# Performance work log

Hardware: AMD Instinct MI355X
Metric: run time of the kernel (lower is better)

The kernel has to match this reference:

```python
import jax, jax.numpy as jnp
import numpy as np

B, C, CI, H, W = 8, 256, 128, 64, 64
STD = 0.01  # conv_init_std
EPS = 1e-5


def setup_inputs() -> dict:
    key = jax.random.key(0)
    ks = jax.random.split(key, 6)
    return {
        "x": jax.random.normal(ks[0], (B, C, H, W), dtype=jnp.float32),
        "theta_w": jax.random.normal(ks[1], (CI, C), dtype=jnp.float32) * STD,
        "theta_b": jnp.zeros((CI,), jnp.float32),
        "phi_w": jax.random.normal(ks[2], (CI, C), dtype=jnp.float32) * STD,
        "phi_b": jnp.zeros((CI,), jnp.float32),
        "g_w": jax.random.normal(ks[3], (CI, C), dtype=jnp.float32) * STD,
        "g_b": jnp.zeros((CI,), jnp.float32),
        "wz_w": jax.random.normal(ks[4], (C, CI), dtype=jnp.float32) * STD,
        "wz_b": jnp.zeros((C,), jnp.float32),
        "bn_gamma": jnp.ones((C,), jnp.float32),
        "bn_beta": jnp.zeros((C,), jnp.float32),
    }


def _conv1x1(x, w, b):
    # 1x1 conv == channel matmul: (B,Cin,H,W),(Cout,Cin) -> (B,Cout,H,W)
    return jnp.einsum('bchw,oc->bohw', x, w) + b[None, :, None, None]


def reference(x, theta_w, theta_b, phi_w, phi_b, g_w, g_b, wz_w, wz_b, bn_gamma, bn_beta):
    b, c, h, w = x.shape
    ci = theta_w.shape[0]
    # query over full resolution: (B, CI, N) with N = H*W
    theta = _conv1x1(x, theta_w, theta_b).reshape(b, ci, h * w)
    # 2x2 maxpool stride 2 for key/value inputs
    xp = x.reshape(b, c, h // 2, 2, w // 2, 2).max(axis=(3, 5))
    phi = _conv1x1(xp, phi_w, phi_b).reshape(b, ci, -1)   # (B, CI, N')
    g = _conv1x1(xp, g_w, g_b).reshape(b, ci, -1)         # (B, CI, N')
    # scaled dot-product attention: scores (B, N, N')
    scores = jnp.einsum('bcn,bcm->bnm', theta, phi) * (ci ** -0.5)
    p = jax.nn.softmax(scores, axis=-1)
    t = jnp.einsum('bcm,bnm->bcn', g, p).reshape(b, ci, h, w)
    z = _conv1x1(t, wz_w, wz_b)
    # BatchNorm2d, training-mode batch statistics (biased variance)
    mean = z.mean(axis=(0, 2, 3))
    var = z.var(axis=(0, 2, 3))
    z = (z - mean[None, :, None, None]) * jax.lax.rsqrt(var + EPS)[None, :, None, None]
    z = z * bn_gamma[None, :, None, None] + bn_beta[None, :, None, None]
    return x + z
```

## Files before the change

### kernel.cpp

```cpp
#include <hip/hip_runtime.h>

#define B_   8
#define C_   256
#define CI_  128
#define HW_  4096
#define HWP_ 1024

typedef short bf16x8 __attribute__((ext_vector_type(8)));
typedef float f32x4 __attribute__((ext_vector_type(4)));
typedef unsigned short u16;
typedef unsigned int u32;

#define SW(row, off) ((off) ^ (((row) & 7) << 4))

__device__ __forceinline__ u16 f2b(float f) {
  u32 u = __builtin_bit_cast(u32, f);
  return (u16)((u + 0x7fffu + ((u >> 16) & 1u)) >> 16);
}
__device__ __forceinline__ u32 cvtpk(float lo, float hi) {
  u32 r;
  asm("v_cvt_pk_bf16_f32 %0, %1, %2" : "=v"(r) : "v"(lo), "v"(hi));
  return r;
}
__device__ __forceinline__ f32x4 mfma16(bf16x8 a, bf16x8 b, f32x4 c) {
  return __builtin_amdgcn_mfma_f32_16x16x32_bf16(a, b, c, 0, 0, 0);
}
__device__ __forceinline__ void gl16(const void* g, void* l) {
  __builtin_amdgcn_global_load_lds(
      (const __attribute__((address_space(1))) u32*)g,
      (__attribute__((address_space(3))) u32*)l, 16, 0, 0);
}

template <int ROWS>
__device__ __forceinline__ void stage_tile(const u16* src, int rstride,
                                           char* lds, int w, int lane) {
#pragma unroll
  for (int it = 0; it < ROWS / 32; ++it) {
    int L = it * 256 + w * 64 + lane;
    int row = L >> 3, slot = L & 7;
    gl16(src + (size_t)row * rstride + ((slot ^ (row & 7)) << 3),
         lds + it * 4096 + w * 1024);
  }
}
__device__ __forceinline__ void stage_tile256(const u16* src, char* lds, int w, int lane) {
#pragma unroll
  for (int it = 0; it < 4; ++it) {
    int L = it * 256 + w * 64 + lane;
    int row = L >> 4, slot = L & 15;
    gl16(src + (size_t)row * 128 + ((slot ^ (row & 7)) << 3),
         lds + it * 4096 + w * 1024);
  }
}

__global__ __launch_bounds__(256) void prep(const float* __restrict__ x,
                                            u16* __restrict__ xt,
                                            u16* __restrict__ xpt,
                                            const float* __restrict__ w0,
                                            const float* __restrict__ w1,
                                            const float* __restrict__ w2,
                                            const float* __restrict__ w3,
                                            u16* __restrict__ wB) {
  const int b = blockIdx.z, p = blockIdx.x;
  const int t = threadIdx.x;
  if (p == 32) {
    if (blockIdx.y == 0 && b < 4) {
      const float* src = (b == 0) ? w0 : (b == 1) ? w1 : (b == 2) ? w2 : w3;
      u16* dst = wB + b * 32768;
      for (int i = t * 8; i < 32768; i += 2048) {
        float4 a = *(const float4*)&src[i];
        float4 c = *(const float4*)&src[i + 4];
        uint4 v;
        v.x = cvtpk(a.x, a.y);
        v.y = cvtpk(a.z, a.w);
        v.z = cvtpk(c.x, c.y);
        v.w = cvtpk(c.z, c.w);
        *(uint4*)&dst[i] = v;
      }
    }
    return;
  }
  __shared__ __align__(16) char sm[16384];
  const int c0 = blockIdx.y * 64;
#pragma unroll
  for (int k = 0; k < 2; ++k) {
    int pi = k * 256 + t;
    int ng = pi & 31, cg = pi >> 5;
    float4 v[4];
#pragma unroll
    for (int cc = 0; cc < 4; ++cc)
      v[cc] = *(const float4*)&x[((size_t)(b * C_ + c0 + cg * 4 + cc)) * HW_ + p * 128 + ng * 4];
#pragma unroll
    for (int jj = 0; jj < 4; ++jj) {
      int n = ng * 4 + jj;
      uint2 pk;
      pk.x = cvtpk(v[0][jj], v[1][jj]);
      pk.y = cvtpk(v[2][jj], v[3][jj]);
      int slot = (cg + ng) & 15;
      *(uint2*)(sm + n * 128 + slot * 8) = pk;
    }
  }
  __syncthreads();
#pragma unroll
  for (int it = 0; it < 4; ++it) {
    int L = it * 256 + t;
    int row = L >> 3, ch = L & 7;
    int s0 = (2 * ch + (row >> 2)) & 15, s1 = (2 * ch + 1 + (row >> 2)) & 15;
    uint2 a = *(const uint2*)(sm + row * 128 + s0 * 8);
    uint2 bb = *(const uint2*)(sm + row * 128 + s1 * 8);
    uint4 o = {a.x, a.y, bb.x, bb.y};
    *(uint4*)(xt + ((size_t)(b * HW_ + p * 128 + row)) * C_ + c0 + ch * 8) = o;
  }
#pragma unroll
  for (int k = 0; k < 2; ++k) {
    int cg = t & 15, mw = (t >> 4) + k * 16;
    int rows[4] = {2 * mw, 2 * mw + 1, 64 + 2 * mw, 65 + 2 * mw};
    uint2 rv[4];
#pragma unroll
    for (int r = 0; r < 4; ++r) {
      int n = rows[r];
      int slot = (cg + (n >> 2)) & 15;
      rv[r] = *(const uint2*)(sm + n * 128 + slot * 8);
    }
    u16 outc[4];
#pragma unroll
    for (int ci = 0; ci < 4; ++ci) {
      float m = -1e30f;
#pragma unroll
      for (int r = 0; r < 4; ++r) {
        u32 word = (ci < 2) ? rv[r].x : rv[r].y;
        u16 h = (u16)((ci & 1) ? (word >> 16) : (word & 0xffff));
        m = fmaxf(m, __builtin_bit_cast(float, (u32)h << 16));
      }
      outc[ci] = (u16)(__builtin_bit_cast(u32, m) >> 16);
    }
    uint2 pk;
    pk.x = (u32)outc[0] | ((u32)outc[1] << 16);
    pk.y = (u32)outc[2] | ((u32)outc[3] << 16);
    *(uint2*)(xpt + ((size_t)(b * HWP_ + p * 32 + mw)) * C_ + c0 + cg * 4) = pk;
  }
}

__global__ __launch_bounds__(256) void gemm_wa(const u16* __restrict__ Wb,
                                               const u16* __restrict__ act,
                                               const float* __restrict__ bias,
                                               u16* __restrict__ outp,
                                               int Ntok) {
  __shared__ __align__(16) char smem[65536];
  const int b = blockIdx.y;
  const int n0 = blockIdx.x * 128;
  const int t = threadIdx.x, lane = t & 63, w = t >> 6;
  const int lr = lane & 15, lg = lane >> 4;
  const int otb = (w & 1) * 4, ntb = (w >> 1) * 4;
  const u16* actb = act + (size_t)(b * Ntok + n0) * 256;
  f32x4 acc[4][4];
#pragma unroll
  for (int i = 0; i < 4; ++i)
#pragma unroll
    for (int j = 0; j < 4; ++j) acc[i][j] = (f32x4){0.f, 0.f, 0.f, 0.f};

  stage_tile<128>(Wb, 256, smem, w, lane);
  stage_tile<128>(actb, 256, smem + 16384, w, lane);
  for (int kc = 0; kc < 4; ++kc) {
    __syncthreads();
    if (kc < 3) {
      char* nb = smem + ((kc + 1) & 1) * 32768;
      stage_tile<128>(Wb + (kc + 1) * 64, 256, nb, w, lane);
      stage_tile<128>(actb + (kc + 1) * 64, 256, nb + 16384, w, lane);
    }
    char* Ws = smem + (kc & 1) * 32768;
    char* Xs = Ws + 16384;
#pragma unroll
    for (int ks = 0; ks < 2; ++ks) {
      bf16x8 af[4], bfr[4];
#pragma unroll
      for (int i = 0; i < 4; ++i) {
        int rA = (otb + i) * 16 + lr;
        af[i] = *(const bf16x8*)(Ws + rA * 128 + SW(rA, ks * 64 + lg * 16));
        int rB = (ntb + i) * 16 + lr;
        bfr[i] = *(const bf16x8*)(Xs + rB * 128 + SW(rB, ks * 64 + lg * 16));
      }
#pragma unroll
      for (int i = 0; i < 4; ++i)
#pragma unroll
        for (int j = 0; j < 4; ++j) acc[i][j] = mfma16(af[i], bfr[j], acc[i][j]);
    }
  }
#pragma unroll
  for (int i = 0; i < 4; ++i) {
    int obase = (otb + i) * 16 + lg * 4;
    float b0 = bias[obase], b1 = bias[obase + 1], b2 = bias[obase + 2], b3 = bias[obase + 3];
#pragma unroll
    for (int j = 0; j < 4; ++j) {
      int n = (ntb + j) * 16 + lr;
      f32x4 v = acc[i][j];
      uint2 pk;
      pk.x = cvtpk(v[0] + b0, v[1] + b1);
      pk.y = cvtpk(v[2] + b2, v[3] + b3);
      *(uint2*)(smem + n * 256 + SW(n, obase * 2)) = pk;
    }
  }
  __syncthreads();
#pragma unroll
  for (int it = 0; it < 8; ++it) {
    int L = it * 256 + t;
    int row = L >> 4, ch = L & 15;
    uint4 v = *(const uint4*)(smem + row * 256 + SW(row, ch * 16));
    *(uint4*)(outp + ((size_t)b * Ntok + n0 + row) * 128 + ch * 8) = v;
  }
}

template <int KD, bool BNP>
__global__ __launch_bounds__(256) void gemm_aw(const u16* __restrict__ act,
                                               const u16* __restrict__ Wb,
                                               const float* __restrict__ bias,
                                               u16* __restrict__ outp,
                                               int Mtok, int O,
                                               float* __restrict__ sums,
                                               float* __restrict__ sqs) {
  __shared__ __align__(16) char smem[49152];
  const int b = blockIdx.z;
  const int m0 = blockIdx.x * 64;
  const int o0 = blockIdx.y * 128;
  const int t = threadIdx.x, lane = t & 63, w = t >> 6;
  const int lr = lane & 15, lg = lane >> 4;
  const int otb = w * 2;
  const u16* actb = act + (size_t)(b * Mtok + m0) * KD;
  const u16* Wbb = Wb + (size_t)o0 * KD;
  constexpr int NCH = KD / 64;
  f32x4 acc[4][2];
#pragma unroll
  for (int i = 0; i < 4; ++i)
#pragma unroll
    for (int j = 0; j < 2; ++j) acc[i][j] = (f32x4){0.f, 0.f, 0.f, 0.f};

  stage_tile<64>(actb, KD, smem, w, lane);
  stage_tile<128>(Wbb, KD, smem + 8192, w, lane);
  for (int kc = 0; kc < NCH; ++kc) {
    __syncthreads();
    if (kc < NCH - 1) {
      char* nb = smem + ((kc + 1) & 1) * 24576;
      stage_tile<64>(actb + (kc + 1) * 64, KD, nb, w, lane);
      stage_tile<128>(Wbb + (kc + 1) * 64, KD, nb + 8192, w, lane);
    }
    char* As = smem + (kc & 1) * 24576;
    char* Bs = As + 8192;
#pragma unroll
    for (int ks = 0; ks < 2; ++ks) {
      bf16x8 af[4], bfr[2];
#pragma unroll
      for (int i = 0; i < 4; ++i) {
        int r = i * 16 + lr;
        af[i] = *(const bf16x8*)(As + r * 128 + SW(r, ks * 64 + lg * 16));
      }
#pragma unroll
      for (int j = 0; j < 2; ++j) {
        int r = (otb + j) * 16 + lr;
        bfr[j] = *(const bf16x8*)(Bs + r * 128 + SW(r, ks * 64 + lg * 16));
      }
#pragma unroll
      for (int i = 0; i < 4; ++i)
#pragma unroll
        for (int j = 0; j < 2; ++j) acc[i][j] = mfma16(af[i], bfr[j], acc[i][j]);
    }
  }
  if (BNP) {
    int pid = blockIdx.z * gridDim.x + blockIdx.x;
#pragma unroll
    for (int j = 0; j < 2; ++j) {
      int o = o0 + (otb + j) * 16 + lr;
      float bi = bias[o];
      float s = 0.f, q = 0.f;
#pragma unroll
      for (int i = 0; i < 4; ++i) {
        f32x4 v = acc[i][j];
#pragma unroll
        for (int r = 0; r < 4; ++r) {
          float vv = v[r] + bi;
          s += vv;
          q += vv * vv;
        }
      }
      s += __shfl_xor(s, 16); q += __shfl_xor(q, 16);
      s += __shfl_xor(s, 32); q += __shfl_xor(q, 32);
      if (lg == 0) {
        sums[(size_t)o * 512 + pid] = s;
        sqs[(size_t)o * 512 + pid] = q;
      }
    }
  }
#pragma unroll
  for (int j = 0; j < 2; ++j) {
    int o = (otb + j) * 16 + lr;
    float bi = bias[o0 + o];
#pragma unroll
    for (int i = 0; i < 4; ++i) {
      int mq = i * 16 + lg * 4;
      f32x4 v = acc[i][j];
      uint2 pk;
      pk.x = cvtpk(v[0] + bi, v[1] + bi);
      pk.y = cvtpk(v[2] + bi, v[3] + bi);
      *(uint2*)(smem + o * 128 + SW(o, mq * 2)) = pk;
    }
  }
  __syncthreads();
#pragma unroll
  for (int it = 0; it < 4; ++it) {
    int L = it * 256 + t;
    int row = L >> 3, ch = L & 7;
    uint4 v = *(const uint4*)(smem + row * 128 + SW(row, ch * 16));
    *(uint4*)(outp + ((size_t)b * O + o0 + row) * Mtok + m0 + ch * 8) = v;
  }
}

#define ATTN_TILE(KCP, WAITV)                                                 \
  {                                                                           \
    const char* Kc = (KCP);                                                   \
    int rn = w * 16 + lr;                                                     \
    _Pragma("unroll")                                                         \
    for (int mt = 0; mt < 4; ++mt) {                                          \
      f32x4 s = {0.f, 0.f, 0.f, 0.f};                                         \
      _Pragma("unroll")                                                       \
      for (int kq = 0; kq < 4; ++kq) {                                        \
        int r = mt * 16 + lr;                                                 \
        bf16x8 a = *(const bf16x8*)(Kc + r * 256 + SW(r, kq * 64 + lg * 16)); \
        s = mfma16(a, qf[kq], s);                                             \
      }                                                                       \
      float p0 = __expf(s[0] * scale), p1 = __expf(s[1] * scale);             \
      float p2 = __expf(s[2] * scale), p3 = __expf(s[3] * scale);             \
      csum += (p0 + p1) + (p2 + p3);                                          \
      uint2 pk;                                                               \
      pk.x = cvtpk(p0, p1);                                                   \
      pk.y = cvtpk(p2, p3);                                                   \
      *(uint2*)(Pn + rn * 128 + SW(rn, mt * 32 + lg * 8)) = pk;               \
    }                                                                         \
    asm volatile("s_waitcnt lgkmcnt(0)" ::: "memory");                        \
    bf16x8 pb0 = *(const bf16x8*)(Pn + rn * 128 + SW(rn, lg * 16));           \
    bf16x8 pb1 = *(const bf16x8*)(Pn + rn * 128 + SW(rn, 64 + lg * 16));      \
    asm volatile("s_waitcnt " WAITV ::: "memory");                            \
    _Pragma("unroll")                                                         \
    for (int ct = 0; ct < 8; ++ct) {                                          \
      int rc = ct * 16 + lr;                                                  \
      bf16x8 a0 = *(const bf16x8*)(Vs + rc * 128 + SW(rc, lg * 16));          \
      bf16x8 a1 = *(const bf16x8*)(Vs + rc * 128 + SW(rc, 64 + lg * 16));     \
      accT[ct] = mfma16(a0, pb0, accT[ct]);                                   \
      accT[ct] = mfma16(a1, pb1, accT[ct]);                                   \
    }                                                                         \
  }

__global__ __launch_bounds__(256) void attn_mfma(const u16* __restrict__ Qt,
                                                 const u16* __restrict__ Kt,
                                                 const u16* __restrict__ Vn,
                                                 u16* __restrict__ Ot) {
  __shared__ __align__(16) char smem[73728];
  char* Vs = smem + 49152;
  char* Pn = smem + 65536;
  const int bid = blockIdx.x;
  const int swz = (bid & 7) * 64 + (bid >> 3);
  const int b = swz >> 6, n0 = (swz & 63) * 64;
  const int t = threadIdx.x, lane = t & 63, w = t >> 6;
  const int lr = lane & 15, lg = lane >> 4;
  const float scale = 0.08838834764831845f;
  const u16* Qbase = Qt + (size_t)(b * HW_ + n0) * 128;
  const u16* Kbase = Kt + (size_t)b * HWP_ * 128;
  const u16* Vbase = Vn + (size_t)b * 128 * HWP_;

  stage_tile256(Qbase, smem, w, lane);
  stage_tile256(Kbase, smem + 16384, w, lane);
  stage_tile<128>(Vbase, HWP_, Vs, w, lane);
  __syncthreads();

  bf16x8 qf[4];
  {
    int r = w * 16 + lr;
#pragma unroll
    for (int kq = 0; kq < 4; ++kq)
      qf[kq] = *(const bf16x8*)(smem + r * 256 + SW(r, kq * 64 + lg * 16));
  }
  f32x4 accT[8];
#pragma unroll
  for (int ct = 0; ct < 8; ++ct) accT[ct] = (f32x4){0.f, 0.f, 0.f, 0.f};
  float csum = 0.f;

  for (int tt = 0; tt < 15; ++tt) {
    stage_tile256(Kbase + (size_t)(tt + 1) * 64 * 128,
                  smem + 16384 + ((tt + 1) & 1) * 16384, w, lane);
    ATTN_TILE(smem + 16384 + (tt & 1) * 16384, "vmcnt(4)");
    __syncthreads();
    stage_tile<128>(Vbase + (tt + 1) * 64, HWP_, Vs, w, lane);
  }
  ATTN_TILE(smem + 16384 + 16384, "vmcnt(0)");

  csum += __shfl_xor(csum, 16);
  csum += __shfl_xor(csum, 32);
  float rinv = 1.f / csum;
  __syncthreads();
  {
    int rn = w * 16 + lr;
#pragma unroll
    for (int ct = 0; ct < 8; ++ct) {
      f32x4 v = accT[ct];
      uint2 pk;
      pk.x = cvtpk(v[0] * rinv, v[1] * rinv);
      pk.y = cvtpk(v[2] * rinv, v[3] * rinv);
      *(uint2*)(smem + 16384 + rn * 256 + SW(rn, ct * 32 + lg * 8)) = pk;
    }
  }
  __syncthreads();
#pragma unroll
  for (int it = 0; it < 4; ++it) {
    int L = it * 256 + t;
    int row = L >> 4, ch = L & 15;
    uint4 v = *(const uint4*)(smem + 16384 + row * 256 + SW(row, ch * 16));
    *(uint4*)(Ot + ((size_t)b * HW_ + n0 + row) * 128 + ch * 8) = v;
  }
}

__global__ __launch_bounds__(256) void bn_finalize(const float* __restrict__ sums,
                                                   const float* __restrict__ sqs,
                                                   float* __restrict__ stats) {
  __shared__ float s1[256], s2[256];
  const int c = blockIdx.x, t = threadIdx.x;
  float a = sums[(size_t)c * 512 + t] + sums[(size_t)c * 512 + 256 + t];
  float q = sqs[(size_t)c * 512 + t] + sqs[(size_t)c * 512 + 256 + t];
  s1[t] = a;
  s2[t] = q;
  __syncthreads();
  for (int st = 128; st > 0; st >>= 1) {
    if (t < st) {
      s1[t] += s1[t + st];
      s2[t] += s2[t + st];
    }
    __syncthreads();
  }
  if (t == 0) {
    const float inv = 1.f / (float)(B_ * HW_);
    float mean = s1[0] * inv;
    float var = s2[0] * inv - mean * mean;
    stats[c] = mean;
    stats[C_ + c] = rsqrtf(var + 1e-5f);
  }
}

__device__ __forceinline__ float blo(u32 u) { return __builtin_bit_cast(float, u << 16); }
__device__ __forceinline__ float bhi(u32 u) { return __builtin_bit_cast(float, u & 0xffff0000u); }

__global__ __launch_bounds__(256) void final8(const float4* __restrict__ x,
                                              const uint4* __restrict__ zb,
                                              const float* __restrict__ stats,
                                              const float* __restrict__ gamma,
                                              const float* __restrict__ beta,
                                              float4* __restrict__ out) {
  size_t i = (size_t)blockIdx.x * 256 + threadIdx.x;
  int c = (int)((i >> 9) & 255);
  float ga = gamma[c] * stats[C_ + c];
  float be = beta[c] - stats[c] * ga;
  uint4 zv = zb[i];
  float4 x0 = x[2 * i], x1 = x[2 * i + 1], o0, o1;
  o0.x = fmaf(blo(zv.x), ga, x0.x + be);
  o0.y = fmaf(bhi(zv.x), ga, x0.y + be);
  o0.z = fmaf(blo(zv.y), ga, x0.z + be);
  o0.w = fmaf(bhi(zv.y), ga, x0.w + be);
  o1.x = fmaf(blo(zv.z), ga, x1.x + be);
  o1.y = fmaf(bhi(zv.z), ga, x1.y + be);
  o1.z = fmaf(blo(zv.w), ga, x1.z + be);
  o1.w = fmaf(bhi(zv.w), ga, x1.w + be);
  out[2 * i] = o0;
  out[2 * i + 1] = o1;
}

extern "C" void kernel_launch(void* const* d_in, const int* in_sizes, int n_in,
                              void* d_out, int out_size, void* d_ws, size_t ws_size,
                              hipStream_t stream) {
  const float* x        = (const float*)d_in[0];
  const float* theta_w  = (const float*)d_in[1];
  const float* theta_b  = (const float*)d_in[2];
  const float* phi_w    = (const float*)d_in[3];
  const float* phi_b    = (const float*)d_in[4];
  const float* g_w      = (const float*)d_in[5];
  const float* g_b      = (const float*)d_in[6];
  const float* wz_w     = (const float*)d_in[7];
  const float* wz_b     = (const float*)d_in[8];
  const float* bn_gamma = (const float*)d_in[9];
  const float* bn_beta  = (const float*)d_in[10];
  float* out = (float*)d_out;

  char* ws = (char*)d_ws;
  u16* x_t     = (u16*)(ws);
  u16* xp_t    = (u16*)(ws + 16777216);
  u16* theta_t = (u16*)(ws + 20971520);
  u16* phi_t   = (u16*)(ws + 29360128);
  u16* g_nat   = (u16*)(ws + 31457280);
  u16* t_t     = (u16*)(ws + 33554432);
  u16* zb      = (u16*)(ws + 41943040);
  float* stats = (float*)(ws + 58720256);
  float* bsums = (float*)(ws + 58722304);
  float* bsqs  = (float*)(ws + 59246592);
  u16* wB      = (u16*)(ws + 59770880);

  prep<<<dim3(33, 4, 8), 256, 0, stream>>>(x, x_t, xp_t, theta_w, phi_w, g_w, wz_w, wB);
  gemm_wa<<<dim3(32, 8), 256, 0, stream>>>(wB, x_t, theta_b, theta_t, HW_);
  gemm_wa<<<dim3(8, 8), 256, 0, stream>>>(wB + 32768, xp_t, phi_b, phi_t, HWP_);
  gemm_aw<256, false><<<dim3(16, 1, 8), 256, 0, stream>>>(
      xp_t, wB + 65536, g_b, g_nat, HWP_, 128, nullptr, nullptr);
  attn_mfma<<<dim3(512), 256, 0, stream>>>(theta_t, phi_t, g_nat, t_t);
  gemm_aw<128, true><<<dim3(64, 2, 8), 256, 0, stream>>>(
      t_t, wB + 98304, wz_b, zb, HW_, 256, bsums, bsqs);
  bn_finalize<<<256, 256, 0, stream>>>(bsums, bsqs, stats);
  final8<<<4096, 256, 0, stream>>>((const float4*)x, (const uint4*)zb, stats,
                                   bn_gamma, bn_beta, (float4*)out);
}
```

Before: 169.1 us.

## Fuse theta projection and output conv with BN partial sums into attention kernel

The theta 1x1 conv is now computed inside the attention kernel from the bf16 x tile staged in LDS. The wz output conv and the per-block BatchNorm partial sums are applied to the attention output while it is still in LDS. This drops two GEMM launches and the global round trips for theta and t. In exchange the attention kernel does more work per block and uses more registers (launch bounds set to 2 blocks per CU), and it reloads weight tiles in every block.

After: 160.1 us. -5.3%, faster.

```diff
diff --git a/kernel.cpp b/kernel.cpp
--- a/kernel.cpp
+++ b/kernel.cpp
@@ -48,6 +48,15 @@
     int L = it * 256 + w * 64 + lane;
     int row = L >> 4, slot = L & 15;
     gl16(src + (size_t)row * 128 + ((slot ^ (row & 7)) << 3),
+         lds + it * 4096 + w * 1024);
+  }
+}
+__device__ __forceinline__ void stage512(const u16* src, char* lds, int w, int lane) {
+#pragma unroll
+  for (int it = 0; it < 8; ++it) {
+    int L = it * 256 + w * 64 + lane;
+    int row = L >> 5, slot = L & 31;
+    gl16(src + (size_t)row * 256 + ((slot ^ (row & 7)) << 3),
          lds + it * 4096 + w * 1024);
   }
 }
@@ -209,14 +218,12 @@
   }
 }
 
-template <int KD, bool BNP>
+template <int KD>
 __global__ __launch_bounds__(256) void gemm_aw(const u16* __restrict__ act,
                                                const u16* __restrict__ Wb,
                                                const float* __restrict__ bias,
                                                u16* __restrict__ outp,
-                                               int Mtok, int O,
-                                               float* __restrict__ sums,
-                                               float* __restrict__ sqs) {
+                                               int Mtok, int O) {
   __shared__ __align__(16) char smem[49152];
   const int b = blockIdx.z;
   const int m0 = blockIdx.x * 64;
@@ -261,31 +268,6 @@
       for (int i = 0; i < 4; ++i)
 #pragma unroll
         for (int j = 0; j < 2; ++j) acc[i][j] = mfma16(af[i], bfr[j], acc[i][j]);
-    }
-  }
-  if (BNP) {
-    int pid = blockIdx.z * gridDim.x + blockIdx.x;
-#pragma unroll
-    for (int j = 0; j < 2; ++j) {
-      int o = o0 + (otb + j) * 16 + lr;
-      float bi = bias[o];
-      float s = 0.f, q = 0.f;
-#pragma unroll
-      for (int i = 0; i < 4; ++i) {
-        f32x4 v = acc[i][j];
-#pragma unroll
-        for (int r = 0; r < 4; ++r) {
-          float vv = v[r] + bi;
-          s += vv;
-          q += vv * vv;
-        }
-      }
-      s += __shfl_xor(s, 16); q += __shfl_xor(q, 16);
-      s += __shfl_xor(s, 32); q += __shfl_xor(q, 32);
-      if (lg == 0) {
-        sums[(size_t)o * 512 + pid] = s;
-        sqs[(size_t)o * 512 + pid] = q;
-      }
     }
   }
 #pragma unroll
@@ -347,11 +329,15 @@
     }                                                                         \
   }
 
-__global__ __launch_bounds__(256) void attn_mfma(const u16* __restrict__ Qt,
-                                                 const u16* __restrict__ Kt,
-                                                 const u16* __restrict__ Vn,
-                                                 u16* __restrict__ Ot) {
+__global__ __launch_bounds__(256, 2) void mega_attn(
+    const u16* __restrict__ xt, const u16* __restrict__ thW,
+    const float* __restrict__ thB, const u16* __restrict__ Kt,
+    const u16* __restrict__ Vn, const u16* __restrict__ wzW,
+    const float* __restrict__ wzB, u16* __restrict__ zb,
+    float* __restrict__ sums, float* __restrict__ sqs) {
   __shared__ __align__(16) char smem[73728];
+  char* Qs = smem;
+  char* KD = smem + 16384;
   char* Vs = smem + 49152;
   char* Pn = smem + 65536;
   const int bid = blockIdx.x;
@@ -360,40 +346,83 @@
   const int t = threadIdx.x, lane = t & 63, w = t >> 6;
   const int lr = lane & 15, lg = lane >> 4;
   const float scale = 0.08838834764831845f;
-  const u16* Qbase = Qt + (size_t)(b * HW_ + n0) * 128;
   const u16* Kbase = Kt + (size_t)b * HWP_ * 128;
   const u16* Vbase = Vn + (size_t)b * 128 * HWP_;
 
-  stage_tile256(Qbase, smem, w, lane);
-  stage_tile256(Kbase, smem + 16384, w, lane);
+  stage512(xt + (size_t)(b * HW_ + n0) * 256, KD, w, lane);
+  stage_tile<128>(thW, 256, Vs, w, lane);
+  f32x4 qacc[2][4];
+#pragma unroll
+  for (int i = 0; i < 2; ++i)
+#pragma unroll
+    for (int j = 0; j < 4; ++j) qacc[i][j] = (f32x4){0.f, 0.f, 0.f, 0.f};
+  for (int kc = 0; kc < 4; ++kc) {
+    __syncthreads();
+#pragma unroll
+    for (int ks = 0; ks < 2; ++ks) {
+      bf16x8 af[2], bx[4];
+#pragma unroll
+      for (int oi = 0; oi < 2; ++oi) {
+        int rA = w * 32 + oi * 16 + lr;
+        af[oi] = *(const bf16x8*)(Vs + rA * 128 + SW(rA, ks * 64 + lg * 16));
+      }
+#pragma unroll
+      for (int nj = 0; nj < 4; ++nj) {
+        int rB = nj * 16 + lr;
+        bx[nj] = *(const bf16x8*)(KD + rB * 512 + SW(rB, kc * 128 + ks * 64 + lg * 16));
+      }
+#pragma unroll
+      for (int oi = 0; oi < 2; ++oi)
+#pragma unroll
+        for (int nj = 0; nj < 4; ++nj)
+          qacc[oi][nj] = mfma16(af[oi], bx[nj], qacc[oi][nj]);
+    }
+    __syncthreads();
+    if (kc < 3) stage_tile<128>(thW + (kc + 1) * 64, 256, Vs, w, lane);
+  }
+#pragma unroll
+  for (int oi = 0; oi < 2; ++oi) {
+    int ob = w * 32 + oi * 16 + lg * 4;
+    float b0 = thB[ob], b1 = thB[ob + 1], b2 = thB[ob + 2], b3 = thB[ob + 3];
+#pragma unroll
+    for (int nj = 0; nj < 4; ++nj) {
+      int n = nj * 16 + lr;
+      f32x4 v = qacc[oi][nj];
+      uint2 pk;
+      pk.x = cvtpk(v[0] + b0, v[1] + b1);
+      pk.y = cvtpk(v[2] + b2, v[3] + b3);
+      *(uint2*)(Qs + n * 256 + SW(n, ob * 2)) = pk;
+    }
+  }
+  __syncthreads();
+
+  stage_tile256(Kbase, KD, w, lane);
   stage_tile<128>(Vbase, HWP_, Vs, w, lane);
-  __syncthreads();
-
   bf16x8 qf[4];
   {
-    int r = w * 16 + lr;
+    int rq = w * 16 + lr;
 #pragma unroll
     for (int kq = 0; kq < 4; ++kq)
-      qf[kq] = *(const bf16x8*)(smem + r * 256 + SW(r, kq * 64 + lg * 16));
+      qf[kq] = *(const bf16x8*)(Qs + rq * 256 + SW(rq, kq * 64 + lg * 16));
   }
   f32x4 accT[8];
 #pragma unroll
   for (int ct = 0; ct < 8; ++ct) accT[ct] = (f32x4){0.f, 0.f, 0.f, 0.f};
   float csum = 0.f;
+  __syncthreads();
 
   for (int tt = 0; tt < 15; ++tt) {
     stage_tile256(Kbase + (size_t)(tt + 1) * 64 * 128,
-                  smem + 16384 + ((tt + 1) & 1) * 16384, w, lane);
-    ATTN_TILE(smem + 16384 + (tt & 1) * 16384, "vmcnt(4)");
+                  KD + ((tt + 1) & 1) * 16384, w, lane);
+    ATTN_TILE(KD + (tt & 1) * 16384, "vmcnt(4)");
     __syncthreads();
     stage_tile<128>(Vbase + (tt + 1) * 64, HWP_, Vs, w, lane);
   }
-  ATTN_TILE(smem + 16384 + 16384, "vmcnt(0)");
+  ATTN_TILE(KD + 16384, "vmcnt(0)");
 
   csum += __shfl_xor(csum, 16);
   csum += __shfl_xor(csum, 32);
   float rinv = 1.f / csum;
-  __syncthreads();
   {
     int rn = w * 16 + lr;
 #pragma unroll
@@ -402,16 +431,84 @@
       uint2 pk;
       pk.x = cvtpk(v[0] * rinv, v[1] * rinv);
       pk.y = cvtpk(v[2] * rinv, v[3] * rinv);
-      *(uint2*)(smem + 16384 + rn * 256 + SW(rn, ct * 32 + lg * 8)) = pk;
-    }
-  }
-  __syncthreads();
-#pragma unroll
-  for (int it = 0; it < 4; ++it) {
+      *(uint2*)(Qs + rn * 256 + SW(rn, ct * 32 + lg * 8)) = pk;
+    }
+  }
+  __syncthreads();
+
+  f32x4 zacc[4][4];
+#pragma unroll
+  for (int i = 0; i < 4; ++i)
+#pragma unroll
+    for (int j = 0; j < 4; ++j) zacc[i][j] = (f32x4){0.f, 0.f, 0.f, 0.f};
+  for (int kc = 0; kc < 2; ++kc) {
+    stage_tile<256>(wzW + kc * 64, 128, KD, w, lane);
+    __syncthreads();
+#pragma unroll
+    for (int ks = 0; ks < 2; ++ks) {
+      bf16x8 at[4], bw[4];
+#pragma unroll
+      for (int ni = 0; ni < 4; ++ni) {
+        int rt = ni * 16 + lr;
+        at[ni] = *(const bf16x8*)(Qs + rt * 256 + SW(rt, kc * 128 + ks * 64 + lg * 16));
+      }
+#pragma unroll
+      for (int oj = 0; oj < 4; ++oj) {
+        int ro = w * 64 + oj * 16 + lr;
+        bw[oj] = *(const bf16x8*)(KD + ro * 128 + SW(ro, ks * 64 + lg * 16));
+      }
+#pragma unroll
+      for (int ni = 0; ni < 4; ++ni)
+#pragma unroll
+        for (int oj = 0; oj < 4; ++oj)
+          zacc[ni][oj] = mfma16(at[ni], bw[oj], zacc[ni][oj]);
+    }
+    __syncthreads();
+  }
+  float bz[4];
+#pragma unroll
+  for (int oj = 0; oj < 4; ++oj) bz[oj] = wzB[w * 64 + oj * 16 + lr];
+#pragma unroll
+  for (int oj = 0; oj < 4; ++oj) {
+    float s = 0.f, q = 0.f;
+#pragma unroll
+    for (int ni = 0; ni < 4; ++ni) {
+      f32x4 v = zacc[ni][oj];
+#pragma unroll
+      for (int r = 0; r < 4; ++r) {
+        float vv = v[r] + bz[oj];
+        s += vv;
+        q += vv * vv;
+      }
+    }
+    s += __shfl_xor(s, 16); q += __shfl_xor(q, 16);
+    s += __shfl_xor(s, 32); q += __shfl_xor(q, 32);
+    if (lg == 0) {
+      int o = w * 64 + oj * 16 + lr;
+      sums[(size_t)o * 512 + swz] = s;
+      sqs[(size_t)o * 512 + swz] = q;
+    }
+  }
+#pragma unroll
+  for (int oj = 0; oj < 4; ++oj) {
+    int o = w * 64 + oj * 16 + lr;
+#pragma unroll
+    for (int ni = 0; ni < 4; ++ni) {
+      int nb = ni * 16 + lg * 4;
+      f32x4 v = zacc[ni][oj];
+      uint2 pk;
+      pk.x = cvtpk(v[0] + bz[oj], v[1] + bz[oj]);
+      pk.y = cvtpk(v[2] + bz[oj], v[3] + bz[oj]);
+      *(uint2*)(KD + o * 128 + SW(o, nb * 2)) = pk;
+    }
+  }
+  __syncthreads();
+#pragma unroll
+  for (int it = 0; it < 8; ++it) {
     int L = it * 256 + t;
-    int row = L >> 4, ch = L & 15;
-    uint4 v = *(const uint4*)(smem + 16384 + row * 256 + SW(row, ch * 16));
-    *(uint4*)(Ot + ((size_t)b * HW_ + n0 + row) * 128 + ch * 8) = v;
+    int row = L >> 3, ch = L & 7;
+    uint4 v = *(const uint4*)(KD + row * 128 + SW(row, ch * 16));
+    *(uint4*)(zb + ((size_t)(b * C_ + row)) * HW_ + n0 + ch * 8) = v;
   }
 }
 
@@ -487,24 +584,19 @@
   char* ws = (char*)d_ws;
   u16* x_t     = (u16*)(ws);
   u16* xp_t    = (u16*)(ws + 16777216);
-  u16* theta_t = (u16*)(ws + 20971520);
-  u16* phi_t   = (u16*)(ws + 29360128);
-  u16* g_nat   = (u16*)(ws + 31457280);
-  u16* t_t     = (u16*)(ws + 33554432);
-  u16* zb      = (u16*)(ws + 41943040);
-  float* stats = (float*)(ws + 58720256);
-  float* bsums = (float*)(ws + 58722304);
-  float* bsqs  = (float*)(ws + 59246592);
-  u16* wB      = (u16*)(ws + 59770880);
+  u16* phi_t   = (u16*)(ws + 20971520);
+  u16* g_nat   = (u16*)(ws + 23068672);
+  u16* zb      = (u16*)(ws + 25165824);
+  float* stats = (float*)(ws + 41943040);
+  float* bsums = (float*)(ws + 41945088);
+  float* bsqs  = (float*)(ws + 42469376);
+  u16* wB      = (u16*)(ws + 42993664);
 
   prep<<<dim3(33, 4, 8), 256, 0, stream>>>(x, x_t, xp_t, theta_w, phi_w, g_w, wz_w, wB);
-  gemm_wa<<<dim3(32, 8), 256, 0, stream>>>(wB, x_t, theta_b, theta_t, HW_);
   gemm_wa<<<dim3(8, 8), 256, 0, stream>>>(wB + 32768, xp_t, phi_b, phi_t, HWP_);
-  gemm_aw<256, false><<<dim3(16, 1, 8), 256, 0, stream>>>(
-      xp_t, wB + 65536, g_b, g_nat, HWP_, 128, nullptr, nullptr);
-  attn_mfma<<<dim3(512), 256, 0, stream>>>(theta_t, phi_t, g_nat, t_t);
-  gemm_aw<128, true><<<dim3(64, 2, 8), 256, 0, stream>>>(
-      t_t, wB + 98304, wz_b, zb, HW_, 256, bsums, bsqs);
+  gemm_aw<256><<<dim3(16, 1, 8), 256, 0, stream>>>(xp_t, wB + 65536, g_b, g_nat, HWP_, 128);
+  mega_attn<<<dim3(512), 256, 0, stream>>>(x_t, wB, theta_b, phi_t, g_nat,
+                                           wB + 98304, wz_b, zb, bsums, bsqs);
   bn_finalize<<<256, 256, 0, stream>>>(bsums, bsqs, stats);
   final8<<<4096, 256, 0, stream>>>((const float4*)x, (const uint4*)zb, stats,
                                    bn_gamma, bn_beta, (float4*)out);
```
